# Kernel tuning notes

Hardware: AMD Instinct MI355X
Metric: run time of the kernel (lower is better)

## Reference

```python
import jax, jax.numpy as jnp
import numpy as np

N, CIN, COUT, T, V, K = 32, 256, 256, 128, 25, 3
BN_EPS = 1e-5


def setup_inputs() -> dict:
    key = jax.random.key(0)
    k0, k1, k2 = jax.random.split(key, 3)
    x = jax.random.normal(k0, (N, CIN, T, V), dtype=jnp.float32)
    A = jax.random.normal(k1, (K, V, V), dtype=jnp.float32)
    W = jax.random.normal(k2, (K * COUT, CIN), dtype=jnp.float32) * 0.02
    b = jnp.zeros((K * COUT,), dtype=jnp.float32)
    gamma = jnp.ones((COUT,), dtype=jnp.float32)
    beta = jnp.zeros((COUT,), dtype=jnp.float32)
    return {"x": x, "A": A, "W": W, "b": b, "gamma": gamma, "beta": beta}


def reference(x, A, W, b, gamma, beta):
    n, c, t, v = x.shape
    k = A.shape[0]
    # 1x1 conv (conv_pos='pre'): [n,c,t,v] x [k*cout, c] -> [n, k*cout, t, v]
    y = jnp.einsum('nctv,oc->notv', x, W) + b[None, :, None, None]
    # split subsets and contract joints against the k adjacency matrices
    y = y.reshape(n, k, -1, t, v)
    y = jnp.einsum('nkctv,kvw->nctw', y, A)
    # BatchNorm2d (training-mode batch stats over n,t,v per channel)
    mu = jnp.mean(y, axis=(0, 2, 3), keepdims=True)
    var = jnp.var(y, axis=(0, 2, 3), keepdims=True)
    yn = (y - mu) * jax.lax.rsqrt(var + BN_EPS)
    out = gamma[None, :, None, None] * yn + beta[None, :, None, None]
    # with_res=False -> residual is 0; ReLU activation
    return jax.nn.relu(out)
```

## Files before the change

### kernel.cpp

```cpp
#include <hip/hip_runtime.h>
#include <cstddef>

#define NN   32
#define CIN  256
#define COUT 256
#define TT   128
#define VV   25
#define KK   3
#define TV   (TT*VV)
#define NTVC (NN*TT*VV)
#define BN_EPS 1e-5f

#define YT_LD 104
#define XS_LD 264

typedef __attribute__((ext_vector_type(8))) short bf16x8;
typedef __attribute__((ext_vector_type(4))) float f32x4;

__device__ __forceinline__ unsigned short f2bf(float f) {
    unsigned int u = __float_as_uint(f);
    u = (u + 0x7fffu + ((u >> 16) & 1u)) >> 16;
    return (unsigned short)u;
}

__device__ __forceinline__ uint2 pk4(f32x4 v) {
    uint2 r;
    asm("v_cvt_pk_bf16_f32 %0, %1, %2" : "=v"(r.x) : "v"(v[0]), "v"(v[1]));
    asm("v_cvt_pk_bf16_f32 %0, %1, %2" : "=v"(r.y) : "v"(v[2]), "v"(v[3]));
    return r;
}

__global__ __launch_bounds__(256)
void convert_w_kernel(const float* __restrict__ W, unsigned short* __restrict__ Wb) {
    int i = blockIdx.x * 256 + threadIdx.x;
    Wb[i] = f2bf(W[i]);
}

__global__ __launch_bounds__(256)
void transpose_x_kernel(const float* __restrict__ x, unsigned short* __restrict__ xT) {
    __shared__ float T[64][65];
    const int n   = blockIdx.z;
    const int s0  = blockIdx.x * 64;
    const int c0  = blockIdx.y * 64;
    const int tid = threadIdx.x;
    const int r    = tid >> 4;
    const int col4 = (tid & 15) * 4;

    const float* xp = x + (size_t)(n * CIN + c0) * TV + s0;
    for (int rr = r; rr < 64; rr += 16) {
        float4 v = *(const float4*)(xp + (size_t)rr * TV + col4);
        T[rr][col4 + 0] = v.x; T[rr][col4 + 1] = v.y;
        T[rr][col4 + 2] = v.z; T[rr][col4 + 3] = v.w;
    }
    __syncthreads();
    unsigned short* op = xT + ((size_t)n * TV + s0) * CIN + c0;
    for (int ss = r; ss < 64; ss += 16) {
        ushort4 o;
        o.x = f2bf(T[col4 + 0][ss]);
        o.y = f2bf(T[col4 + 1][ss]);
        o.z = f2bf(T[col4 + 2][ss]);
        o.w = f2bf(T[col4 + 3][ss]);
        *(ushort4*)(op + (size_t)ss * CIN + col4) = o;
    }
}

__global__ __launch_bounds__(512, 2)
void gemm_adj_kernel(const unsigned short* __restrict__ xT,
                     const unsigned short* __restrict__ Wb,
                     const float* __restrict__ A,
                     const float* __restrict__ b,
                     float* __restrict__ y2,
                     float* __restrict__ statsN)
{
    __shared__ __align__(16) unsigned short U[CIN * YT_LD];
    __shared__ __align__(16) unsigned short Ab[32 * 96];

    const int tid  = threadIdx.x;
    const int lane = tid & 63;
    const int wg   = tid >> 6;
    const int ln15 = lane & 15;
    const int quad = lane >> 4;
    const int tp   = blockIdx.x & 63;
    const int n    = blockIdx.x >> 6;
    const int t0   = tp * 2;

    {
        const unsigned short* xsrc = xT + ((size_t)n * TV + (size_t)t0 * VV) * CIN;
        for (int ch = tid; ch < 1600; ch += 512) {
            const int s = ch >> 5, c8 = ch & 31;
            *(bf16x8*)&U[s * XS_LD + c8 * 8] = *(const bf16x8*)&xsrc[ch * 8];
        }
        const bf16x8 z = {0,0,0,0,0,0,0,0};
        for (int ch = tid; ch < 231; ch += 512) {
            const int s = 50 + ch / 33, c8 = ch - (ch / 33) * 33;
            *(bf16x8*)&U[s * XS_LD + c8 * 8] = z;
        }
        for (int i = tid; i < 32 * 96; i += 512) {
            const int w = i / 96, kv = i - w * 96;
            const int k = kv >> 5, v = kv & 31;
            const float val = (v < VV && w < VV) ? A[k * VV * VV + v * VV + w] : 0.f;
            Ab[i] = f2bf(val);
        }
    }

    f32x4 acc[4][6];
    #pragma unroll
    for (int nt = 0; nt < 6; ++nt) {
        const float bv = b[96 * wg + 16 * nt + ln15];
        #pragma unroll
        for (int mt = 0; mt < 4; ++mt)
            #pragma unroll
            for (int r = 0; r < 4; ++r)
                acc[mt][nt][r] = bv;
    }

    __syncthreads();

    const int soff[4] = {0, 16, 25, 41};
    const unsigned short* wp = Wb + (size_t)(96 * wg + ln15) * CIN + quad * 8;
    bf16x8 wbuf[2][6];
    #pragma unroll
    for (int nt = 0; nt < 6; ++nt)
        wbuf[0][nt] = *(const bf16x8*)(wp + (size_t)nt * 16 * CIN);

    #pragma unroll
    for (int ks = 0; ks < 8; ++ks) {
        const int cur = ks & 1, nxt = cur ^ 1;
        if (ks < 7) {
            #pragma unroll
            for (int nt = 0; nt < 6; ++nt)
                wbuf[nxt][nt] = *(const bf16x8*)(wp + (size_t)nt * 16 * CIN + (ks + 1) * 32);
        }
        bf16x8 xfr[4];
        #pragma unroll
        for (int mt = 0; mt < 4; ++mt)
            xfr[mt] = *(const bf16x8*)&U[(soff[mt] + ln15) * XS_LD + ks * 32 + quad * 8];
        #pragma unroll
        for (int mt = 0; mt < 4; ++mt)
            #pragma unroll
            for (int nt = 0; nt < 6; ++nt)
                acc[mt][nt] = __builtin_amdgcn_mfma_f32_16x16x32_bf16(
                                  xfr[mt], wbuf[cur][nt], acc[mt][nt], 0, 0, 0);
    }

    __syncthreads();

    for (int i = tid; i < CIN * 21; i += 512) {
        const int c = i / 21, rr = i - c * 21;
        const int k = rr / 7, v = VV + (rr - k * 7);
        U[c * YT_LD + k * 32 + v] = 0;
    }

    const int obase = 96 * wg + ln15;

    auto write_half = [&](int h) {
        const int mtF = 2 * h, mtP = 2 * h + 1;
        {
            const int v0 = quad * 4;
            #pragma unroll
            for (int nt = 0; nt < 6; ++nt) {
                const int o = obase + 16 * nt;
                *(uint2*)&U[(o & 255) * YT_LD + (o >> 8) * 32 + v0] = pk4(acc[mtF][nt]);
            }
        }
        if (quad < 2) {
            const int v0 = 16 + quad * 4;
            #pragma unroll
            for (int nt = 0; nt < 6; ++nt) {
                const int o = obase + 16 * nt;
                *(uint2*)&U[(o & 255) * YT_LD + (o >> 8) * 32 + v0] = pk4(acc[mtP][nt]);
            }
        } else if (quad == 2) {
            #pragma unroll
            for (int nt = 0; nt < 6; ++nt) {
                const int o = obase + 16 * nt;
                U[(o & 255) * YT_LD + (o >> 8) * 32 + 24] = f2bf(acc[mtP][nt][0]);
            }
        }
    };

    bf16x8 bq[3][2];
    float bsum1[2][4], bsum2[2][4];
    #pragma unroll
    for (int it = 0; it < 2; ++it)
        #pragma unroll
        for (int r = 0; r < 4; ++r) { bsum1[it][r] = 0.f; bsum2[it][r] = 0.f; }

    #pragma unroll
    for (int h = 0; h < 2; ++h) {
        if (h) __syncthreads();
        write_half(h);
        __syncthreads();

        if (h == 0) {
            #pragma unroll
            for (int k = 0; k < 3; ++k)
                #pragma unroll
                for (int nw = 0; nw < 2; ++nw)
                    bq[k][nw] = *(const bf16x8*)&Ab[(16 * nw + ln15) * 96 + k * 32 + quad * 8];
        }

        #pragma unroll
        for (int it = 0; it < 2; ++it) {
            const int cb = (wg * 2 + it) * 16;
            f32x4 a2[2];
            #pragma unroll
            for (int nw = 0; nw < 2; ++nw)
                #pragma unroll
                for (int r = 0; r < 4; ++r) a2[nw][r] = 0.f;
            #pragma unroll
            for (int k = 0; k < 3; ++k) {
                const bf16x8 af = *(const bf16x8*)&U[(cb + ln15) * YT_LD + k * 32 + quad * 8];
                a2[0] = __builtin_amdgcn_mfma_f32_16x16x32_bf16(af, bq[k][0], a2[0], 0, 0, 0);
                a2[1] = __builtin_amdgcn_mfma_f32_16x16x32_bf16(af, bq[k][1], a2[1], 0, 0, 0);
            }
            const int t = t0 + h;
            float* op = y2 + (size_t)n * COUT * TV
                           + (size_t)(cb + 4 * quad) * TV + (size_t)t * VV;
            #pragma unroll
            for (int r = 0; r < 4; ++r) {
                const float va = a2[0][r];
                const float vb = a2[1][r];
                op[r * TV + ln15] = va;
                if (ln15 < 9) op[r * TV + 16 + ln15] = vb;
                const float vbm = (ln15 < 9) ? vb : 0.f;
                bsum1[it][r] += va + vbm;
                bsum2[it][r] += va * va + vbm * vbm;
            }
        }
    }

    #pragma unroll
    for (int it = 0; it < 2; ++it)
        #pragma unroll
        for (int r = 0; r < 4; ++r) {
            float s1 = bsum1[it][r], s2 = bsum2[it][r];
            #pragma unroll
            for (int off = 1; off < 16; off <<= 1) {
                s1 += __shfl_xor(s1, off);
                s2 += __shfl_xor(s2, off);
            }
            if (ln15 == 0) {
                const int c = (wg * 2 + it) * 16 + quad * 4 + r;
                atomicAdd(&statsN[n * 512 + c], s1);
                atomicAdd(&statsN[n * 512 + 256 + c], s2);
            }
        }
}

__global__ void bn_stats_kernel(const float* __restrict__ statsN,
                                const float* __restrict__ gamma,
                                const float* __restrict__ beta,
                                float* __restrict__ ss)
{
    int c = threadIdx.x;
    float s1 = 0.f, s2 = 0.f;
    for (int g = 0; g < NN; ++g) {
        s1 += statsN[g * 512 + c];
        s2 += statsN[g * 512 + 256 + c];
    }
    float mu  = s1 * (1.f / NTVC);
    float var = s2 * (1.f / NTVC) - mu * mu;
    float sc  = gamma[c] * rsqrtf(var + BN_EPS);
    ss[c]        = sc;
    ss[COUT + c] = beta[c] - mu * sc;
}

__global__ __launch_bounds__(256)
void bn_apply_kernel(float* __restrict__ y, const float* __restrict__ ss)
{
    int i = blockIdx.x * 256 + threadIdx.x;
    int f = i * 4;
    int cch = (f / TV) & (COUT - 1);
    float sc = ss[cch], sh = ss[COUT + cch];
    float4 v = ((float4*)y)[i];
    v.x = fmaxf(v.x * sc + sh, 0.f);
    v.y = fmaxf(v.y * sc + sh, 0.f);
    v.z = fmaxf(v.z * sc + sh, 0.f);
    v.w = fmaxf(v.w * sc + sh, 0.f);
    ((float4*)y)[i] = v;
}

extern "C" void kernel_launch(void* const* d_in, const int* in_sizes, int n_in,
                              void* d_out, int out_size, void* d_ws, size_t ws_size,
                              hipStream_t stream)
{
    const float* x     = (const float*)d_in[0];
    const float* A     = (const float*)d_in[1];
    const float* W     = (const float*)d_in[2];
    const float* b     = (const float*)d_in[3];
    const float* gamma = (const float*)d_in[4];
    const float* beta  = (const float*)d_in[5];
    float* out = (float*)d_out;

    float* statsN = (float*)d_ws;
    float* ss     = (float*)((char*)d_ws + 65536);
    unsigned short* Wb  = (unsigned short*)((char*)d_ws + 67584);
    unsigned short* xTb = (unsigned short*)((char*)d_ws + 67584 + (size_t)KK * COUT * CIN * 2);

    hipMemsetAsync(statsN, 0, (size_t)NN * 512 * sizeof(float), stream);

    convert_w_kernel<<<(KK * COUT * CIN) / 256, 256, 0, stream>>>(W, Wb);
    transpose_x_kernel<<<dim3(TV / 64, CIN / 64, NN), 256, 0, stream>>>(x, xTb);
    gemm_adj_kernel<<<NN * (TT / 2), 512, 0, stream>>>(xTb, Wb, A, b, out, statsN);
    bn_stats_kernel<<<1, 256, 0, stream>>>(statsN, gamma, beta, ss);
    bn_apply_kernel<<<(NN * COUT * TT * VV) / (4 * 256), 256, 0, stream>>>(out, ss);
}
```

Baseline: 395.8 us.

## Double gemm_adj block to 1024 threads, halving per-wave output tile

```diff
diff --git a/kernel.cpp b/kernel.cpp
--- a/kernel.cpp
+++ b/kernel.cpp
@@ -64,7 +64,7 @@
     }
 }
 
-__global__ __launch_bounds__(512, 2)
+__global__ __launch_bounds__(1024)
 void gemm_adj_kernel(const unsigned short* __restrict__ xT,
                      const unsigned short* __restrict__ Wb,
                      const float* __restrict__ A,
@@ -86,27 +86,26 @@
 
     {
         const unsigned short* xsrc = xT + ((size_t)n * TV + (size_t)t0 * VV) * CIN;
-        for (int ch = tid; ch < 1600; ch += 512) {
+        for (int ch = tid; ch < 1600; ch += 1024) {
             const int s = ch >> 5, c8 = ch & 31;
             *(bf16x8*)&U[s * XS_LD + c8 * 8] = *(const bf16x8*)&xsrc[ch * 8];
         }
         const bf16x8 z = {0,0,0,0,0,0,0,0};
-        for (int ch = tid; ch < 231; ch += 512) {
-            const int s = 50 + ch / 33, c8 = ch - (ch / 33) * 33;
-            *(bf16x8*)&U[s * XS_LD + c8 * 8] = z;
-        }
-        for (int i = tid; i < 32 * 96; i += 512) {
+        for (int ch = tid; ch < 231; ch += 1024) {
+            const int rr = 50 + ch / 33, c8 = ch - (ch / 33) * 33;
+            *(bf16x8*)&U[rr * XS_LD + c8 * 8] = z;
+        }
+        for (int i = tid; i < 32 * 96; i += 1024) {
             const int w = i / 96, kv = i - w * 96;
             const int k = kv >> 5, v = kv & 31;
-            const float val = (v < VV && w < VV) ? A[k * VV * VV + v * VV + w] : 0.f;
-            Ab[i] = f2bf(val);
-        }
-    }
-
-    f32x4 acc[4][6];
-    #pragma unroll
-    for (int nt = 0; nt < 6; ++nt) {
-        const float bv = b[96 * wg + 16 * nt + ln15];
+            Ab[i] = f2bf((v < VV && w < VV) ? A[k * VV * VV + v * VV + w] : 0.f);
+        }
+    }
+
+    f32x4 acc[4][3];
+    #pragma unroll
+    for (int nt = 0; nt < 3; ++nt) {
+        const float bv = b[48 * wg + 16 * nt + ln15];
         #pragma unroll
         for (int mt = 0; mt < 4; ++mt)
             #pragma unroll
@@ -117,10 +116,10 @@
     __syncthreads();
 
     const int soff[4] = {0, 16, 25, 41};
-    const unsigned short* wp = Wb + (size_t)(96 * wg + ln15) * CIN + quad * 8;
-    bf16x8 wbuf[2][6];
-    #pragma unroll
-    for (int nt = 0; nt < 6; ++nt)
+    const unsigned short* wp = Wb + (size_t)(48 * wg + ln15) * CIN + quad * 8;
+    bf16x8 wbuf[2][3];
+    #pragma unroll
+    for (int nt = 0; nt < 3; ++nt)
         wbuf[0][nt] = *(const bf16x8*)(wp + (size_t)nt * 16 * CIN);
 
     #pragma unroll
@@ -128,7 +127,7 @@
         const int cur = ks & 1, nxt = cur ^ 1;
         if (ks < 7) {
             #pragma unroll
-            for (int nt = 0; nt < 6; ++nt)
+            for (int nt = 0; nt < 3; ++nt)
                 wbuf[nxt][nt] = *(const bf16x8*)(wp + (size_t)nt * 16 * CIN + (ks + 1) * 32);
         }
         bf16x8 xfr[4];
@@ -138,27 +137,27 @@
         #pragma unroll
         for (int mt = 0; mt < 4; ++mt)
             #pragma unroll
-            for (int nt = 0; nt < 6; ++nt)
+            for (int nt = 0; nt < 3; ++nt)
                 acc[mt][nt] = __builtin_amdgcn_mfma_f32_16x16x32_bf16(
                                   xfr[mt], wbuf[cur][nt], acc[mt][nt], 0, 0, 0);
     }
 
     __syncthreads();
 
-    for (int i = tid; i < CIN * 21; i += 512) {
+    for (int i = tid; i < CIN * 21; i += 1024) {
         const int c = i / 21, rr = i - c * 21;
         const int k = rr / 7, v = VV + (rr - k * 7);
         U[c * YT_LD + k * 32 + v] = 0;
     }
 
-    const int obase = 96 * wg + ln15;
+    const int obase = 48 * wg + ln15;
 
     auto write_half = [&](int h) {
         const int mtF = 2 * h, mtP = 2 * h + 1;
         {
             const int v0 = quad * 4;
             #pragma unroll
-            for (int nt = 0; nt < 6; ++nt) {
+            for (int nt = 0; nt < 3; ++nt) {
                 const int o = obase + 16 * nt;
                 *(uint2*)&U[(o & 255) * YT_LD + (o >> 8) * 32 + v0] = pk4(acc[mtF][nt]);
             }
@@ -166,13 +165,13 @@
         if (quad < 2) {
             const int v0 = 16 + quad * 4;
             #pragma unroll
-            for (int nt = 0; nt < 6; ++nt) {
+            for (int nt = 0; nt < 3; ++nt) {
                 const int o = obase + 16 * nt;
                 *(uint2*)&U[(o & 255) * YT_LD + (o >> 8) * 32 + v0] = pk4(acc[mtP][nt]);
             }
         } else if (quad == 2) {
             #pragma unroll
-            for (int nt = 0; nt < 6; ++nt) {
+            for (int nt = 0; nt < 3; ++nt) {
                 const int o = obase + 16 * nt;
                 U[(o & 255) * YT_LD + (o >> 8) * 32 + 24] = f2bf(acc[mtP][nt][0]);
             }
@@ -180,11 +179,10 @@
     };
 
     bf16x8 bq[3][2];
-    float bsum1[2][4], bsum2[2][4];
-    #pragma unroll
-    for (int it = 0; it < 2; ++it)
-        #pragma unroll
-        for (int r = 0; r < 4; ++r) { bsum1[it][r] = 0.f; bsum2[it][r] = 0.f; }
+    float bsum1[4], bsum2[4];
+    #pragma unroll
+    for (int r = 0; r < 4; ++r) { bsum1[r] = 0.f; bsum2[r] = 0.f; }
+    const int cb = wg * 16;
 
     #pragma unroll
     for (int h = 0; h < 2; ++h) {
@@ -200,52 +198,46 @@
                     bq[k][nw] = *(const bf16x8*)&Ab[(16 * nw + ln15) * 96 + k * 32 + quad * 8];
         }
 
-        #pragma unroll
-        for (int it = 0; it < 2; ++it) {
-            const int cb = (wg * 2 + it) * 16;
-            f32x4 a2[2];
-            #pragma unroll
-            for (int nw = 0; nw < 2; ++nw)
-                #pragma unroll
-                for (int r = 0; r < 4; ++r) a2[nw][r] = 0.f;
-            #pragma unroll
-            for (int k = 0; k < 3; ++k) {
-                const bf16x8 af = *(const bf16x8*)&U[(cb + ln15) * YT_LD + k * 32 + quad * 8];
-                a2[0] = __builtin_amdgcn_mfma_f32_16x16x32_bf16(af, bq[k][0], a2[0], 0, 0, 0);
-                a2[1] = __builtin_amdgcn_mfma_f32_16x16x32_bf16(af, bq[k][1], a2[1], 0, 0, 0);
-            }
-            const int t = t0 + h;
-            float* op = y2 + (size_t)n * COUT * TV
-                           + (size_t)(cb + 4 * quad) * TV + (size_t)t * VV;
-            #pragma unroll
-            for (int r = 0; r < 4; ++r) {
-                const float va = a2[0][r];
-                const float vb = a2[1][r];
-                op[r * TV + ln15] = va;
-                if (ln15 < 9) op[r * TV + 16 + ln15] = vb;
-                const float vbm = (ln15 < 9) ? vb : 0.f;
-                bsum1[it][r] += va + vbm;
-                bsum2[it][r] += va * va + vbm * vbm;
-            }
-        }
-    }
-
-    #pragma unroll
-    for (int it = 0; it < 2; ++it)
+        f32x4 a2[2];
+        #pragma unroll
+        for (int nw = 0; nw < 2; ++nw)
+            #pragma unroll
+            for (int r = 0; r < 4; ++r) a2[nw][r] = 0.f;
+        #pragma unroll
+        for (int k = 0; k < 3; ++k) {
+            const bf16x8 af = *(const bf16x8*)&U[(cb + ln15) * YT_LD + k * 32 + quad * 8];
+            a2[0] = __builtin_amdgcn_mfma_f32_16x16x32_bf16(af, bq[k][0], a2[0], 0, 0, 0);
+            a2[1] = __builtin_amdgcn_mfma_f32_16x16x32_bf16(af, bq[k][1], a2[1], 0, 0, 0);
+        }
+        const int t = t0 + h;
+        float* op = y2 + (size_t)n * COUT * TV
+                       + (size_t)(cb + 4 * quad) * TV + (size_t)t * VV;
         #pragma unroll
         for (int r = 0; r < 4; ++r) {
-            float s1 = bsum1[it][r], s2 = bsum2[it][r];
-            #pragma unroll
-            for (int off = 1; off < 16; off <<= 1) {
-                s1 += __shfl_xor(s1, off);
-                s2 += __shfl_xor(s2, off);
-            }
-            if (ln15 == 0) {
-                const int c = (wg * 2 + it) * 16 + quad * 4 + r;
-                atomicAdd(&statsN[n * 512 + c], s1);
-                atomicAdd(&statsN[n * 512 + 256 + c], s2);
-            }
-        }
+            const float va = a2[0][r];
+            const float vb = a2[1][r];
+            op[r * TV + ln15] = va;
+            if (ln15 < 9) op[r * TV + 16 + ln15] = vb;
+            const float vbm = (ln15 < 9) ? vb : 0.f;
+            bsum1[r] += va + vbm;
+            bsum2[r] += va * va + vbm * vbm;
+        }
+    }
+
+    #pragma unroll
+    for (int r = 0; r < 4; ++r) {
+        float s1 = bsum1[r], s2 = bsum2[r];
+        #pragma unroll
+        for (int off = 1; off < 16; off <<= 1) {
+            s1 += __shfl_xor(s1, off);
+            s2 += __shfl_xor(s2, off);
+        }
+        if (ln15 == 0) {
+            const int c = cb + 4 * quad + r;
+            atomicAdd(&statsN[n * 512 + c], s1);
+            atomicAdd(&statsN[n * 512 + 256 + c], s2);
+        }
+    }
 }
 
 __global__ void bn_stats_kernel(const float* __restrict__ statsN,
@@ -302,7 +294,7 @@
 
     convert_w_kernel<<<(KK * COUT * CIN) / 256, 256, 0, stream>>>(W, Wb);
     transpose_x_kernel<<<dim3(TV / 64, CIN / 64, NN), 256, 0, stream>>>(x, xTb);
-    gemm_adj_kernel<<<NN * (TT / 2), 512, 0, stream>>>(xTb, Wb, A, b, out, statsN);
+    gemm_adj_kernel<<<NN * (TT / 2), 1024, 0, stream>>>(xTb, Wb, A, b, out, statsN);
     bn_stats_kernel<<<1, 256, 0, stream>>>(statsN, gamma, beta, ss);
     bn_apply_kernel<<<(NN * COUT * TT * VV) / (4 * 256), 256, 0, stream>>>(out, ss);
 }
```

Result: faster. 386.1 us (-2.4%).
